# Kernel optimization log

Measured on AMD Instinct MI355X. Metric: run time of the kernel, lower is better.

## Reference

```python
import jax, jax.numpy as jnp
import numpy as np

E = 1024      # embed_dim
H = 16        # num_heads
D = E // H    # head_dim = 64
K = 4         # num_hyper_nodes
MAX_SEQ = 8192
ROPE_BASE = 10000.0
SCALE = D ** -0.5


def rotate_half(x):
    half = x.shape[-1] // 2
    return jnp.concatenate([-x[..., half:], x[..., :half]], axis=-1)


def _rope_cache():
    inv_freq = 1.0 / (ROPE_BASE ** (jnp.arange(0, D, 2, dtype=jnp.float32) / D))
    t = jnp.arange(MAX_SEQ, dtype=jnp.float32)
    freqs = jnp.outer(t, inv_freq)                       # (MAX_SEQ, D/2)
    emb = jnp.concatenate([freqs, freqs], axis=-1)       # (MAX_SEQ, D)
    return jnp.cos(emb), jnp.sin(emb)


def setup_inputs() -> dict:
    key = jax.random.key(0)
    ks = jax.random.split(key, 6)
    B, S = 2, 2048
    w_scale = E ** -0.5  # keep pre-softmax logits in a sane range
    return {
        "x":  jax.random.normal(ks[0], (B, S, E), dtype=jnp.float32),
        "Wq": jax.random.normal(ks[1], (E, E), dtype=jnp.float32) * w_scale,
        "Wk": jax.random.normal(ks[2], (E, E), dtype=jnp.float32) * w_scale,
        "Wv": jax.random.normal(ks[3], (E, E), dtype=jnp.float32) * w_scale,
        "Wr": jax.random.normal(ks[4], (E, H * K), dtype=jnp.float32) * w_scale,
        "Wo": jax.random.normal(ks[5], (E, E), dtype=jnp.float32) * w_scale,
    }


def reference(x, Wq, Wk, Wv, Wr, Wo):
    B, S, _ = x.shape
    # projections -> (B, H, S, D)
    q = (x @ Wq).reshape(B, S, H, D).transpose(0, 2, 1, 3)
    k = (x @ Wk).reshape(B, S, H, D).transpose(0, 2, 1, 3)
    v = (x @ Wv).reshape(B, S, H, D).transpose(0, 2, 1, 3)

    # node routing probabilities (B, H, S, K)
    logits = (x @ Wr).reshape(B, S, H, K).transpose(0, 2, 1, 3)
    node_probs = jax.nn.softmax(logits, axis=-1)

    # expected per-node position: sum_{j<i} p[j,k]  -> (B, H, S, K)
    expected_pos = jnp.cumsum(node_probs, axis=2) - node_probs

    # fractional-position RoPE via linear interpolation of the cos/sin cache
    cos_c, sin_c = _rope_cache()
    pos = jnp.clip(expected_pos, 0.0, MAX_SEQ - 1)
    pf = pos.astype(jnp.int32)                   # floor
    pc = jnp.minimum(pf + 1, MAX_SEQ - 1)        # ceil
    frac = (pos - pf.astype(pos.dtype))[..., None]
    cos = cos_c[pf] + frac * (cos_c[pc] - cos_c[pf])   # (B,H,S,K,D)
    sin = sin_c[pf] + frac * (sin_c[pc] - sin_c[pf])

    # Weighted combine over nodes. Since q_k = q*cos_k + rh(q)*sin_k is linear
    # in (cos_k, sin_k), sum_k p_k * q_k = q * (sum_k p_k cos_k) + rh(q) * (sum_k p_k sin_k)
    cos_w = jnp.einsum('bhsk,bhskd->bhsd', node_probs, cos)
    sin_w = jnp.einsum('bhsk,bhskd->bhsd', node_probs, sin)
    q_r = q * cos_w + rotate_half(q) * sin_w
    k_r = k * cos_w + rotate_half(k) * sin_w

    # P(same node) weights (B, H, S, S)
    node_w = jnp.einsum('bhik,bhjk->bhij', node_probs, node_probs)

    scores = jnp.einsum('bhid,bhjd->bhij', q_r, k_r) * SCALE
    scores = scores + jnp.log(node_w + 1e-8)
    causal = jnp.tril(jnp.ones((S, S), dtype=bool))
    scores = jnp.where(causal[None, None], scores, -jnp.inf)
    attn = jax.nn.softmax(scores, axis=-1)

    out = jnp.einsum('bhij,bhjd->bhid', attn, v)
    out = out.transpose(0, 2, 1, 3).reshape(B, S, E)
    return out @ Wo
```

## Files before the change

kernel.cpp:

```cpp
#include <hip/hip_runtime.h>

#define E_ 1024
#define H_ 16
#define D_ 64
#define K_ 4
#define S_ 2048
#define B_ 2
#define BS_ 4096
#define BH_ 32
#define CT_ 2080

typedef __attribute__((ext_vector_type(8))) short short8;
typedef __attribute__((ext_vector_type(4))) float f32x4;
typedef __attribute__((ext_vector_type(4))) unsigned short u16x4;

__device__ __forceinline__ unsigned short f2bf(float f) {
  union { float f; unsigned u; } v; v.f = f;
  unsigned r = v.u + 0x7FFFu + ((v.u >> 16) & 1u);
  return (unsigned short)(r >> 16);
}
__device__ __forceinline__ float bf2f(unsigned short u) {
  union { unsigned u; float f; } v; v.u = ((unsigned)u) << 16; return v.f;
}

typedef __attribute__((address_space(1))) const void gvoid;
typedef __attribute__((address_space(3))) void lvoid;
__device__ __forceinline__ void gload_lds16(const void* g, void* l) {
  __builtin_amdgcn_global_load_lds((gvoid*)g, (lvoid*)l, 16, 0, 0);
}

__device__ __forceinline__ short8 lds8(const unsigned short* base, int row, int chunk) {
  int off = row * 128 + (((chunk ^ (row & 7)) & 7) << 4);
  return *(const short8*)((const char*)base + off);
}

__device__ __forceinline__ float redmax16(float v) {
  int iv = __float_as_int(v);
  v = fmaxf(v, __int_as_float(__builtin_amdgcn_update_dpp(iv, iv, 0xB1, 0xF, 0xF, true)));
  iv = __float_as_int(v);
  v = fmaxf(v, __int_as_float(__builtin_amdgcn_update_dpp(iv, iv, 0x4E, 0xF, 0xF, true)));
  v = fmaxf(v, __shfl_xor(v, 4, 16));
  v = fmaxf(v, __shfl_xor(v, 8, 16));
  return v;
}

__global__ __launch_bounds__(256) void k_prep(const float* __restrict__ x,
    const float* __restrict__ Wq, const float* __restrict__ Wk, const float* __restrict__ Wv,
    const float* __restrict__ Wo, const float* __restrict__ Wr,
    unsigned short* __restrict__ xb, unsigned short* __restrict__ wt,
    float* __restrict__ cosc, float* __restrict__ sinc, float* __restrict__ logits) {
  __shared__ __align__(16) char smem[40960];
  int blk = blockIdx.x;
  int t = threadIdx.x;

  if (blk < 4096) {
    int i = blk * 256 + t;
    float4 v = ((const float4*)x)[i];
    u16x4 o; o.x = f2bf(v.x); o.y = f2bf(v.y); o.z = f2bf(v.z); o.w = f2bf(v.w);
    ((u16x4*)xb)[i] = o;
    return;
  }
  blk -= 4096;
  if (blk < 1024) {
    int z = blk >> 8, rem = blk & 255;
    int k0 = (rem >> 4) * 64, n0 = (rem & 15) * 64;
    const float* W = z == 0 ? Wq : z == 1 ? Wk : z == 2 ? Wv : Wo;
    unsigned short* out = wt + (size_t)z * E_ * E_;
    float (*tile)[65] = (float(*)[65])smem;
    int r = t >> 2, q4 = t & 3;
#pragma unroll
    for (int q = 0; q < 4; q++) {
      int c4 = q4 + q * 4;
      float4 v = *(const float4*)&W[(size_t)(k0 + r) * E_ + n0 + c4 * 4];
      tile[r][c4 * 4 + 0] = v.x; tile[r][c4 * 4 + 1] = v.y;
      tile[r][c4 * 4 + 2] = v.z; tile[r][c4 * 4 + 3] = v.w;
    }
    __syncthreads();
#pragma unroll
    for (int q = 0; q < 4; q++) {
      int cb = (q4 + q * 4) * 4;
      u16x4 o;
      o.x = f2bf(tile[cb + 0][r]); o.y = f2bf(tile[cb + 1][r]);
      o.z = f2bf(tile[cb + 2][r]); o.w = f2bf(tile[cb + 3][r]);
      *(u16x4*)&out[(size_t)(n0 + r) * E_ + k0 + cb] = o;
    }
    return;
  }
  blk -= 1024;
  if (blk < 260) {
    int i = blk * 256 + t;
    if (i < CT_ * 32) {
      int tt = i >> 5, f = i & 31;
      float invf = __expf(-(float)(2 * f) * (9.210340371976184f / 64.f));
      float ang = (float)tt * invf;
      cosc[i] = cosf(ang); sinc[i] = sinf(ang);
    }
    return;
  }
  blk -= 260;
  {
    float* xs = (float*)smem;
    float* ws = xs + 2048;
    int m0 = blk * 16;
    int r = t >> 4, cq = t & 15;
    f32x4 acc = {0.f, 0.f, 0.f, 0.f};

    auto stage = [&](int chunk, int buf) {
      int e0 = chunk * 64;
      gload_lds16(x + (size_t)(m0 + (t >> 4)) * E_ + e0 + (((t & 15) ^ (t >> 4)) << 2),
                  xs + buf * 1024 + t * 4);
#pragma unroll
      for (int j = 0; j < 4; j++) {
        int slot = j * 256 + t;
        gload_lds16(Wr + (size_t)(e0 + (slot >> 4)) * 64 + ((slot & 15) << 2),
                    ws + buf * 4096 + slot * 4);
      }
    };

    stage(0, 0);
    __syncthreads();
    for (int chunk = 0; chunk < 16; chunk++) {
      int cur = chunk & 1;
      if (chunk < 15) stage(chunk + 1, cur ^ 1);
#pragma unroll
      for (int e4 = 0; e4 < 16; e4++) {
        f32x4 xf = *(const f32x4*)(xs + cur * 1024 + (r * 16 + (e4 ^ r)) * 4);
#pragma unroll
        for (int i = 0; i < 4; i++) {
          f32x4 wf = *(const f32x4*)(ws + cur * 4096 + ((e4 * 4 + i) * 16 + cq) * 4);
          acc[0] = fmaf(xf[i], wf[0], acc[0]);
          acc[1] = fmaf(xf[i], wf[1], acc[1]);
          acc[2] = fmaf(xf[i], wf[2], acc[2]);
          acc[3] = fmaf(xf[i], wf[3], acc[3]);
        }
      }
      __syncthreads();
    }
    *(f32x4*)&logits[(size_t)(m0 + r) * 64 + cq * 4] = acc;
  }
}

__global__ __launch_bounds__(256) void k_scan1(const float* __restrict__ logits,
    float* __restrict__ probs, unsigned short* __restrict__ pb, float* __restrict__ eposl,
    float* __restrict__ chunkSum) {
  int g = blockIdx.x;
  int bh = g >> 3, c = g & 7;
  int b = bh >> 4, h = bh & 15;
  int t = threadIdx.x;
  int s = c * 256 + t;
  float4 lg = *(const float4*)&logits[(size_t)(b * S_ + s) * 64 + h * 4];
  float m = fmaxf(fmaxf(lg.x, lg.y), fmaxf(lg.z, lg.w));
  float e0 = __expf(lg.x - m), e1 = __expf(lg.y - m), e2 = __expf(lg.z - m), e3 = __expf(lg.w - m);
  float inv = 1.f / (e0 + e1 + e2 + e3);
  float p[4] = {e0 * inv, e1 * inv, e2 * inv, e3 * inv};
  float4 pv; pv.x = p[0]; pv.y = p[1]; pv.z = p[2]; pv.w = p[3];
  *(float4*)&probs[((size_t)bh * S_ + s) * 4] = pv;
  u16x4 pu; pu.x = f2bf(p[0]); pu.y = f2bf(p[1]); pu.z = f2bf(p[2]); pu.w = f2bf(p[3]);
  *(u16x4*)&pb[((size_t)bh * S_ + s) * 4] = pu;

  __shared__ float sc[4][256];
#pragma unroll
  for (int k = 0; k < 4; k++) sc[k][t] = p[k];
  __syncthreads();
  for (int off = 1; off < 256; off <<= 1) {
    float v0 = 0, v1 = 0, v2 = 0, v3 = 0;
    if (t >= off) { v0 = sc[0][t - off]; v1 = sc[1][t - off]; v2 = sc[2][t - off]; v3 = sc[3][t - off]; }
    __syncthreads();
    if (t >= off) { sc[0][t] += v0; sc[1][t] += v1; sc[2][t] += v2; sc[3][t] += v3; }
    __syncthreads();
  }
  float4 ev;
  ev.x = sc[0][t] - p[0]; ev.y = sc[1][t] - p[1];
  ev.z = sc[2][t] - p[2]; ev.w = sc[3][t] - p[3];
  *(float4*)&eposl[((size_t)bh * S_ + s) * 4] = ev;
  if (t == 255) {
    float4 cs; cs.x = sc[0][255]; cs.y = sc[1][255]; cs.z = sc[2][255]; cs.w = sc[3][255];
    *(float4*)&chunkSum[(size_t)(bh * 8 + c) * 4] = cs;
  }
}

__global__ __launch_bounds__(64) void k_scan2(const float* __restrict__ chunkSum,
    float* __restrict__ chunkBase) {
  int bh = threadIdx.x;
  if (bh >= 32) return;
  float r0 = 0.f, r1 = 0.f, r2 = 0.f, r3 = 0.f;
  for (int c = 0; c < 8; c++) {
    float4 cs = *(const float4*)&chunkSum[(size_t)(bh * 8 + c) * 4];
    float4 cb; cb.x = r0; cb.y = r1; cb.z = r2; cb.w = r3;
    *(float4*)&chunkBase[(size_t)(bh * 8 + c) * 4] = cb;
    r0 += cs.x; r1 += cs.y; r2 += cs.z; r3 += cs.w;
  }
}

__global__ __launch_bounds__(256) void k_cwsw(const float* __restrict__ probs,
    const float* __restrict__ eposl, const float* __restrict__ chunkBase,
    const float* __restrict__ cosc, const float* __restrict__ sinc,
    float* __restrict__ cw, float* __restrict__ sw) {
  int bh = blockIdx.y;
  int s = blockIdx.x * 8 + (threadIdx.x >> 5);
  int f = threadIdx.x & 31;
  size_t row = (size_t)bh * S_ + s;
  const float* cb = &chunkBase[(size_t)(bh * 8 + (s >> 8)) * 4];
  float cacc = 0.f, sacc = 0.f;
#pragma unroll
  for (int k = 0; k < 4; k++) {
    float pk = probs[row * 4 + k];
    float pos = eposl[row * 4 + k] + cb[k];
    pos = fminf(fmaxf(pos, 0.f), (float)(CT_ - 2));
    int pf = (int)pos; float fr = pos - (float)pf;
    float c0 = cosc[pf * 32 + f], c1 = cosc[pf * 32 + 32 + f];
    float s0 = sinc[pf * 32 + f], s1 = sinc[pf * 32 + 32 + f];
    cacc = fmaf(pk, c0 + fr * (c1 - c0), cacc);
    sacc = fmaf(pk, s0 + fr * (s1 - s0), sacc);
  }
  cw[row * 32 + f] = cacc; sw[row * 32 + f] = sacc;
}

__device__ __forceinline__ void gemm_128x128(const unsigned short* __restrict__ A,
    const unsigned short* __restrict__ Bt, int m0, int n0,
    unsigned short* lA, unsigned short* lB, f32x4 acc[4][4]) {
  int t = threadIdx.x, w = t >> 6, lane = t & 63;
  int wm = w >> 1, wn = w & 1;
  int arow = lane & 15, agrp = lane >> 4;
  for (int k0 = 0; k0 < E_; k0 += 64) {
    __syncthreads();
#pragma unroll
    for (int j = 0; j < 4; j++) {
      int c = j * 256 + w * 64 + lane;
      int row = c >> 3, slot = c & 7;
      gload_lds16(A + (size_t)(m0 + row) * E_ + k0 + ((slot ^ (row & 7)) << 3),
                  lA + (size_t)(j * 256 + w * 64) * 8);
      gload_lds16(Bt + (size_t)(n0 + row) * E_ + k0 + ((slot ^ (row & 7)) << 3),
                  lB + (size_t)(j * 256 + w * 64) * 8);
    }
    __syncthreads();
#pragma unroll
    for (int ks = 0; ks < 2; ks++) {
      short8 af[4], bfr[4];
#pragma unroll
      for (int mi = 0; mi < 4; mi++) af[mi] = lds8(lA, wm * 64 + mi * 16 + arow, ks * 4 + agrp);
#pragma unroll
      for (int nj = 0; nj < 4; nj++) bfr[nj] = lds8(lB, wn * 64 + nj * 16 + arow, ks * 4 + agrp);
#pragma unroll
      for (int mi = 0; mi < 4; mi++)
#pragma unroll
        for (int nj = 0; nj < 4; nj++)
          acc[mi][nj] = __builtin_amdgcn_mfma_f32_16x16x32_bf16(af[mi], bfr[nj], acc[mi][nj], 0, 0, 0);
    }
  }
}

__global__ __launch_bounds__(256) void k_gemm_qkv(const unsigned short* __restrict__ xb,
    const unsigned short* __restrict__ wt, const float* __restrict__ cw, const float* __restrict__ sw,
    unsigned short* __restrict__ qr, unsigned short* __restrict__ kr, unsigned short* __restrict__ vb) {
  __shared__ unsigned short lA[128 * 64], lB[128 * 64];
  int z = blockIdx.z;
  int m0 = blockIdx.y * 128, n0 = blockIdx.x * 128;
  f32x4 acc[4][4];
  f32x4 zero4 = {0.f, 0.f, 0.f, 0.f};
#pragma unroll
  for (int a = 0; a < 4; a++)
#pragma unroll
    for (int b2 = 0; b2 < 4; b2++) acc[a][b2] = zero4;
  gemm_128x128(xb, wt + (size_t)z * E_ * E_, m0, n0, lA, lB, acc);

  int t = threadIdx.x, w = t >> 6, lane = t & 63;
  int wm = w >> 1, wn = w & 1;
  int arow = lane & 15, agrp = lane >> 4;
  if (z == 2) {
#pragma unroll
    for (int mi = 0; mi < 4; mi++) {
      int i0 = m0 + wm * 64 + mi * 16 + agrp * 4;
      int b = i0 >> 11, s0 = i0 & 2047;
#pragma unroll
      for (int nj = 0; nj < 4; nj++) {
        int col = n0 + wn * 64 + nj * 16 + arow;
        int h = col >> 6, dl = col & 63;
        u16x4 o;
        o.x = f2bf(acc[mi][nj][0]); o.y = f2bf(acc[mi][nj][1]);
        o.z = f2bf(acc[mi][nj][2]); o.w = f2bf(acc[mi][nj][3]);
        *(u16x4*)&vb[((size_t)(b * H_ + h) * 64 + dl) * S_ + s0] = o;
      }
    }
  } else {
    unsigned short* out = (z == 0) ? qr : kr;
    float scl = (z == 0) ? 0.18033688011f : 1.0f;
    int h = (n0 + wn * 64) >> 6;
#pragma unroll
    for (int mi = 0; mi < 4; mi++)
#pragma unroll
      for (int reg = 0; reg < 4; reg++) {
        int i = m0 + wm * 64 + mi * 16 + agrp * 4 + reg;
        int b = i >> 11, s = i & 2047;
        size_t rbase = (size_t)(b * H_ + h) * S_ + s;
        float cw0 = cw[rbase * 32 + arow], cw1 = cw[rbase * 32 + 16 + arow];
        float sw0 = sw[rbase * 32 + arow], sw1 = sw[rbase * 32 + 16 + arow];
#pragma unroll
        for (int nj = 0; nj < 4; nj++) {
          float v = acc[mi][nj][reg];
          float part = acc[mi][nj ^ 2][reg];
          float rh = (nj < 2) ? -part : part;
          float cwv = (nj & 1) ? cw1 : cw0;
          float swv = (nj & 1) ? sw1 : sw0;
          out[rbase * 64 + nj * 16 + arow] = f2bf((v * cwv + rh * swv) * scl);
        }
      }
  }
}

__global__ __launch_bounds__(256) void k_gemm_out(const unsigned short* __restrict__ ob,
    const unsigned short* __restrict__ wot, float* __restrict__ dout) {
  __shared__ unsigned short lA[64 * 64];
  __shared__ unsigned short lB[128 * 64];
  int m0 = blockIdx.y * 64, n0 = blockIdx.x * 128;
  int t = threadIdx.x, w = t >> 6, lane = t & 63;
  int arow = lane & 15, agrp = lane >> 4;
  f32x4 acc[4][2];
  f32x4 zero4 = {0.f, 0.f, 0.f, 0.f};
#pragma unroll
  for (int a = 0; a < 4; a++) { acc[a][0] = zero4; acc[a][1] = zero4; }
  for (int k0 = 0; k0 < E_; k0 += 64) {
    __syncthreads();
#pragma unroll
    for (int j = 0; j < 2; j++) {
      int c = j * 256 + t;
      int row = c >> 3, slot = c & 7;
      gload_lds16(ob + (size_t)(m0 + row) * E_ + k0 + ((slot ^ (row & 7)) << 3),
                  lA + (size_t)c * 8);
    }
#pragma unroll
    for (int j = 0; j < 4; j++) {
      int c = j * 256 + t;
      int row = c >> 3, slot = c & 7;
      gload_lds16(wot + (size_t)(n0 + row) * E_ + k0 + ((slot ^ (row & 7)) << 3),
                  lB + (size_t)c * 8);
    }
    __syncthreads();
#pragma unroll
    for (int ks = 0; ks < 2; ks++) {
      short8 af[4], bfr[2];
#pragma unroll
      for (int mi = 0; mi < 4; mi++) af[mi] = lds8(lA, mi * 16 + arow, ks * 4 + agrp);
#pragma unroll
      for (int nj = 0; nj < 2; nj++) bfr[nj] = lds8(lB, w * 32 + nj * 16 + arow, ks * 4 + agrp);
#pragma unroll
      for (int mi = 0; mi < 4; mi++)
#pragma unroll
        for (int nj = 0; nj < 2; nj++)
          acc[mi][nj] = __builtin_amdgcn_mfma_f32_16x16x32_bf16(af[mi], bfr[nj], acc[mi][nj], 0, 0, 0);
    }
  }
#pragma unroll
  for (int mi = 0; mi < 4; mi++)
#pragma unroll
    for (int reg = 0; reg < 4; reg++) {
      int i = m0 + mi * 16 + agrp * 4 + reg;
#pragma unroll
      for (int nj = 0; nj < 2; nj++) {
        int col = n0 + w * 32 + nj * 16 + arow;
        dout[(size_t)i * E_ + col] = acc[mi][nj][reg];
      }
    }
}

__device__ const int4 kChunk[38] = {
  { 8,0, 8, 8},{ 8,9,17, 9},{12,0, 8,19},{12,9,17,20},
  { 7,0, 7, 6},{ 7,8,15, 7},{10,0, 7,13},{11,0, 7,16},{11,8,15,17},{11,16,23,18},
  {12,18,25,21},{14,0, 7,26},{14,8,15,27},{15,0, 7,30},{15,8,15,31},{15,16,23,32},
  {15,24,31,33},{ 3,0, 7,-1},
  { 6,0, 6, 4},{ 6,7,13, 5},{ 9,0, 6,10},{ 9,7,13,11},{10,8,14,14},{10,15,21,15},
  {13,0, 6,22},{13,7,13,23},{13,14,20,24},{13,21,27,25},{14,16,22,28},{14,23,29,29},
  { 5,0, 5, 2},{ 5,6,11, 3},{ 9,14,19,12},{ 2,0, 5,-1},
  { 4,0, 4, 0},{ 4,5, 9, 1},{ 1,0, 3,-1},{ 0,0, 1,-1}
};

__device__ __forceinline__ short8 mkfrag(u16x4 pv) {
  union { u16x4 v; unsigned u[2]; } pun; pun.v = pv;
  union { short8 s; unsigned u[4]; } z;
  z.u[0] = pun.u[0]; z.u[1] = pun.u[1]; z.u[2] = 0; z.u[3] = 0;
  return z.s;
}

__device__ __forceinline__ void qk_phase2(const char* lKc, const short8 qf[2][2],
    const int kOff[2][4], f32x4 zero4, f32x4 sacc[2][4]) {
#pragma unroll
  for (int ct = 0; ct < 4; ct++) {
    short8 kf = *(const short8*)(lKc + kOff[0][ct]);
    sacc[0][ct] = __builtin_amdgcn_mfma_f32_16x16x32_bf16(qf[0][0], kf, zero4, 0, 0, 0);
    sacc[1][ct] = __builtin_amdgcn_mfma_f32_16x16x32_bf16(qf[1][0], kf, zero4, 0, 0, 0);
  }
#pragma unroll
  for (int ct = 0; ct < 4; ct++) {
    short8 kf = *(const short8*)(lKc + kOff[1][ct]);
    sacc[0][ct] = __builtin_amdgcn_mfma_f32_16x16x32_bf16(qf[0][1], kf, sacc[0][ct], 0, 0, 0);
    sacc[1][ct] = __builtin_amdgcn_mfma_f32_16x16x32_bf16(qf[1][1], kf, sacc[1][ct], 0, 0, 0);
  }
}

__device__ __forceinline__ void softmax_half(const f32x4 sacc[4], const short8 piF,
    const short8 pjF[4], char* lPh, int kv0, int ig_base, int arow, int agrp,
    const int wOff[4][4], float mrow[4], f32x4 oacc[4], f32x4& o4) {
  f32x4 eps4 = {1e-8f, 1e-8f, 1e-8f, 1e-8f};
  f32x4 nwa[4];
#pragma unroll
  for (int ct = 0; ct < 4; ct++)
    nwa[ct] = __builtin_amdgcn_mfma_f32_16x16x32_bf16(piF, pjF[ct], eps4, 0, 0, 0);
  float sv[4][4];
  float rmax[4];
  if (kv0 + 63 > ig_base) {
#pragma unroll
    for (int ct = 0; ct < 4; ct++) {
      int jg = kv0 + ct * 16 + arow;
#pragma unroll
      for (int reg = 0; reg < 4; reg++) {
        int ig = ig_base + agrp * 4 + reg;
        float xv = sacc[ct][reg];
        if (jg > ig) xv = -1e30f;
        sv[ct][reg] = xv;
      }
    }
  } else {
#pragma unroll
    for (int ct = 0; ct < 4; ct++)
#pragma unroll
      for (int reg = 0; reg < 4; reg++)
        sv[ct][reg] = sacc[ct][reg];
  }
#pragma unroll
  for (int reg = 0; reg < 4; reg++)
    rmax[reg] = redmax16(fmaxf(fmaxf(sv[0][reg], sv[1][reg]), fmaxf(sv[2][reg], sv[3][reg])));
  bool ok = (rmax[0] <= mrow[0] + 11.5f) & (rmax[1] <= mrow[1] + 11.5f) &
            (rmax[2] <= mrow[2] + 11.5f) & (rmax[3] <= mrow[3] + 11.5f);
  if (!__all(ok)) {
    float alpha[4];
#pragma unroll
    for (int reg = 0; reg < 4; reg++) {
      float mn = fmaxf(mrow[reg], rmax[reg]);
      alpha[reg] = __builtin_amdgcn_exp2f(mrow[reg] - mn);
      mrow[reg] = mn;
    }
#pragma unroll
    for (int dt = 0; dt < 4; dt++) {
      f32x4 o = oacc[dt];
      o.x *= alpha[0]; o.y *= alpha[1]; o.z *= alpha[2]; o.w *= alpha[3];
      oacc[dt] = o;
    }
    o4.x *= alpha[0]; o4.y *= alpha[1]; o4.z *= alpha[2]; o4.w *= alpha[3];
  }
#pragma unroll
  for (int ct = 0; ct < 4; ct++)
#pragma unroll
    for (int reg = 0; reg < 4; reg++)
      sv[ct][reg] = __builtin_amdgcn_exp2f(sv[ct][reg] - mrow[reg]) * nwa[ct][reg];
#pragma unroll
  for (int ct = 0; ct < 4; ct++) {
#pragma unroll
    for (int rp = 0; rp < 2; rp++) {
      unsigned pk;
      asm("v_cvt_pk_bf16_f32 %0, %1, %2" : "=v"(pk) : "v"(sv[ct][rp * 2]), "v"(sv[ct][rp * 2 + 1]));
      *(unsigned short*)(lPh + wOff[ct][rp * 2 + 0]) = (unsigned short)pk;
      *(unsigned short*)(lPh + wOff[ct][rp * 2 + 1]) = (unsigned short)(pk >> 16);
    }
  }
}

__device__ __forceinline__ void pv2(const char* lPw, const char* lVc,
    const int pOff[2], const int kOff[2][4], f32x4 oacc0[4], f32x4 oacc1[4],
    f32x4& o40, f32x4& o41) {
  const short8 ones = {16256, 16256, 16256, 16256, 16256, 16256, 16256, 16256};
#pragma unroll
  for (int ks = 0; ks < 2; ks++) {
    short8 pf0 = *(const short8*)(lPw + pOff[ks]);
    short8 pf1 = *(const short8*)(lPw + 2048 + pOff[ks]);
    o40 = __builtin_amdgcn_mfma_f32_16x16x32_bf16(pf0, ones, o40, 0, 0, 0);
    o41 = __builtin_amdgcn_mfma_f32_16x16x32_bf16(pf1, ones, o41, 0, 0, 0);
#pragma unroll
    for (int dt = 0; dt < 4; dt++) {
      short8 vf = *(const short8*)(lVc + kOff[ks][dt]);
      oacc0[dt] = __builtin_amdgcn_mfma_f32_16x16x32_bf16(pf0, vf, oacc0[dt], 0, 0, 0);
      oacc1[dt] = __builtin_amdgcn_mfma_f32_16x16x32_bf16(pf1, vf, oacc1[dt], 0, 0, 0);
    }
  }
}

__global__ __launch_bounds__(256, 2) void k_attn(const unsigned short* __restrict__ qr,
    const unsigned short* __restrict__ kr, const unsigned short* __restrict__ vb,
    const unsigned short* __restrict__ pb, unsigned short* __restrict__ ob,
    unsigned short* __restrict__ ObP, float* __restrict__ ml) {
  __shared__ unsigned short lK[2][64 * 64];
  __shared__ unsigned short lV[2][64 * 64];
  __shared__ unsigned short lP[4][2][16 * 64];
  int id = blockIdx.x;
  int xcd = id & 7, slt = id >> 3;
  int bh = xcd * 4 + (slt & 3);
  int4 ck = kChunk[slt >> 2];
  int qt2 = ck.x, j0 = ck.y, j1 = ck.z, part = ck.w;
  int t = threadIdx.x, w = t >> 6, lane = t & 63;
  int arow = lane & 15, agrp = lane >> 4;
  int q0 = qt2 * 128;
  size_t base = (size_t)bh * S_ * 64;
  size_t bhS = (size_t)bh * S_;

  int kOff[2][4], pOff[2], wOff[4][4];
#pragma unroll
  for (int ks = 0; ks < 2; ks++) {
    pOff[ks] = arow * 128 + (((ks * 4 + agrp) ^ (arow & 7)) << 4);
#pragma unroll
    for (int ct = 0; ct < 4; ct++) {
      int row = ct * 16 + arow;
      kOff[ks][ct] = row * 128 + (((ks * 4 + agrp) ^ (row & 7)) << 4);
    }
  }
#pragma unroll
  for (int ct = 0; ct < 4; ct++) {
    int col2 = (ct * 16 + arow) * 2;
#pragma unroll
    for (int rr = 0; rr < 4; rr++) {
      int r = agrp * 4 + rr;
      wOff[ct][rr] = r * 128 + (col2 ^ ((r & 7) << 4));
    }
  }

  const unsigned short* kSrc[2];
  const unsigned short* vSrc[2];
  unsigned short* kDst[2];
  unsigned short* vDst[2];
#pragma unroll
  for (int j = 0; j < 2; j++) {
    int c = j * 256 + w * 64 + lane;
    int row = c >> 3, slot = c & 7;
    kSrc[j] = kr + base + (size_t)row * 64 + ((slot ^ (row & 7)) << 3);
    vSrc[j] = vb + base + (size_t)row * S_ + ((slot ^ (row & 7)) << 3);
    kDst[j] = &lK[0][(j * 256 + w * 64) * 8];
    vDst[j] = &lV[0][(j * 256 + w * 64) * 8];
  }
  const unsigned short* pjSrc[4];
#pragma unroll
  for (int ct = 0; ct < 4; ct++) pjSrc[ct] = pb + (bhS + ct * 16 + arow) * 4;

  short8 qf[2][2];
  short8 piF[2];
  float mrow[2][4];
  f32x4 oacc[2][4];
  f32x4 o4[2];
  f32x4 zero4 = {0.f, 0.f, 0.f, 0.f};
#pragma unroll
  for (int hh = 0; hh < 2; hh++) {
#pragma unroll
    for (int ks = 0; ks < 2; ks++)
      qf[hh][ks] = *(const short8*)&qr[base + (size_t)(q0 + hh * 64 + w * 16 + arow) * 64 + ks * 32 + agrp * 8];
    u16x4 pv = {0, 0, 0, 0};
    if (agrp == 0) pv = *(const u16x4*)&pb[(bhS + q0 + hh * 64 + w * 16 + arow) * 4];
    piF[hh] = mkfrag(pv);
#pragma unroll
    for (int reg = 0; reg < 4; reg++) mrow[hh][reg] = -1e30f;
#pragma unroll
    for (int dt = 0; dt < 4; dt++) oacc[hh][dt] = zero4;
    o4[hh] = zero4;
  }

  auto stageK = [&](int jt, int buf) {
#pragma unroll
    for (int j = 0; j < 2; j++)
      gload_lds16(kSrc[j] + jt * 4096, kDst[j] + buf * 4096);
  };
  auto stageV = [&](int jt, int buf) {
#pragma unroll
    for (int j = 0; j < 2; j++)
      gload_lds16(vSrc[j] + jt * 64, vDst[j] + buf * 4096);
  };
  auto loadPj = [&](int jt, u16x4 pj[4]) {
#pragma unroll
    for (int ct = 0; ct < 4; ct++) {
      u16x4 z = {0, 0, 0, 0};
      if (agrp == 0) z = *(const u16x4*)(pjSrc[ct] + jt * 256);
      pj[ct] = z;
    }
  };

  u16x4 pjv[4], pjvn[4];
  stageK(j0, 0);
  stageV(j0, 0);
  loadPj(j0, pjv);
  __syncthreads();

  char* lPw = (char*)&lP[w][0][0];
  int nt = j1 - j0 + 1;
  for (int i = 0; i < nt; i++) {
    int cur = i & 1;
    int kv0 = (j0 + i) * 64;
    bool hn = (i + 1) < nt;
    if (hn) {
      stageK(j0 + i + 1, cur ^ 1);
      stageV(j0 + i + 1, cur ^ 1);
    }

    f32x4 sacc[2][4];
    __builtin_amdgcn_s_setprio(1);
    qk_phase2((const char*)lK + cur * 8192, qf, kOff, zero4, sacc);
    __builtin_amdgcn_s_setprio(0);

    short8 pjF[4];
#pragma unroll
    for (int ct = 0; ct < 4; ct++) pjF[ct] = mkfrag(pjv[ct]);
#pragma unroll
    for (int hh = 0; hh < 2; hh++)
      softmax_half(sacc[hh], piF[hh], pjF, lPw + hh * 2048, kv0, q0 + hh * 64 + w * 16,
                   arow, agrp, wOff, mrow[hh], oacc[hh], o4[hh]);

    if (hn) loadPj(j0 + i + 1, pjvn);

    asm volatile("s_waitcnt lgkmcnt(0)" ::: "memory");
    __builtin_amdgcn_sched_barrier(0);
    __builtin_amdgcn_s_setprio(1);
    pv2(lPw, (const char*)lV + cur * 8192, pOff, kOff, oacc[0], oacc[1], o4[0], o4[1]);
    __builtin_amdgcn_s_setprio(0);
    if (hn) {
#pragma unroll
      for (int ct = 0; ct < 4; ct++) pjv[ct] = pjvn[ct];
    }
    __syncthreads();
  }

  if (part >= 0) {
    unsigned short* Op = ObP + ((size_t)bh * 34 + part) * 8192;
    float* mlp = ml + ((size_t)bh * 34 + part) * 256;
#pragma unroll
    for (int hh = 0; hh < 2; hh++) {
#pragma unroll
      for (int dt = 0; dt < 4; dt++)
#pragma unroll
        for (int reg = 0; reg < 4; reg++) {
          int row = hh * 64 + w * 16 + agrp * 4 + reg;
          Op[row * 64 + dt * 16 + arow] = f2bf(oacc[hh][dt][reg]);
        }
      if (arow == 0) {
#pragma unroll
        for (int reg = 0; reg < 4; reg++) {
          int row = hh * 64 + w * 16 + agrp * 4 + reg;
          mlp[row] = mrow[hh][reg];
          mlp[128 + row] = o4[hh][reg];
        }
      }
    }
  } else {
    int b = bh >> 4, h8 = bh & 15;
#pragma unroll
    for (int hh = 0; hh < 2; hh++) {
      f32x4 inv4;
      inv4.x = 1.f / o4[hh].x; inv4.y = 1.f / o4[hh].y;
      inv4.z = 1.f / o4[hh].z; inv4.w = 1.f / o4[hh].w;
#pragma unroll
      for (int dt = 0; dt < 4; dt++)
#pragma unroll
        for (int reg = 0; reg < 4; reg++) {
          int i = q0 + hh * 64 + w * 16 + agrp * 4 + reg;
          int d = dt * 16 + arow;
          float v = oacc[hh][dt][reg] * inv4[reg];
          ob[((size_t)(b * S_ + i) * H_ + h8) * 64 + d] = f2bf(v);
        }
    }
  }
}

__global__ __launch_bounds__(256) void k_merge(const unsigned short* __restrict__ ObP,
    const float* __restrict__ ml, unsigned short* __restrict__ ob) {
  int qx = blockIdx.x, bh = blockIdx.y;
  int qt2 = 4 + qx;
  int np = qt2 <= 8 ? 2 : (qt2 <= 12 ? 3 : 4);
  int bslot = qt2 <= 8 ? (qt2 - 4) * 2 : (qt2 <= 12 ? 10 + (qt2 - 9) * 3 : 22 + (qt2 - 13) * 4);
  int t = threadIdx.x;
  int r = t >> 1, dh = (t & 1) * 32;
  float mp[4], lp[4];
  float m = -1e30f;
  for (int p2 = 0; p2 < np; p2++) {
    const float* mlp = ml + ((size_t)bh * 34 + bslot + p2) * 256;
    mp[p2] = mlp[r]; lp[p2] = mlp[128 + r];
    m = fmaxf(m, mp[p2]);
  }
  float a[4], l = 0.f;
  for (int p2 = 0; p2 < np; p2++) { a[p2] = __builtin_amdgcn_exp2f(mp[p2] - m); l = fmaf(lp[p2], a[p2], l); }
  float inv = 1.f / l;
  for (int p2 = 0; p2 < np; p2++) a[p2] *= inv;
  int i = qt2 * 128 + r, b = bh >> 4, h = bh & 15;
  unsigned short* op = ob + ((size_t)(b * S_ + i) * H_ + h) * 64 + dh;
#pragma unroll
  for (int q = 0; q < 8; q++) {
    float a0 = 0.f, a1 = 0.f, a2 = 0.f, a3 = 0.f;
    for (int p2 = 0; p2 < np; p2++) {
      const unsigned short* Op = ObP + ((size_t)bh * 34 + bslot + p2) * 8192 + r * 64 + dh + q * 4;
      u16x4 xx = *(const u16x4*)Op;
      a0 = fmaf(bf2f(xx.x), a[p2], a0);
      a1 = fmaf(bf2f(xx.y), a[p2], a1);
      a2 = fmaf(bf2f(xx.z), a[p2], a2);
      a3 = fmaf(bf2f(xx.w), a[p2], a3);
    }
    u16x4 o; o.x = f2bf(a0); o.y = f2bf(a1); o.z = f2bf(a2); o.w = f2bf(a3);
    *(u16x4*)(op + q * 4) = o;
  }
}

extern "C" void kernel_launch(void* const* d_in, const int* in_sizes, int n_in,
                              void* d_out, int out_size, void* d_ws, size_t ws_size,
                              hipStream_t stream) {
  const float* x  = (const float*)d_in[0];
  const float* Wq = (const float*)d_in[1];
  const float* Wk = (const float*)d_in[2];
  const float* Wv = (const float*)d_in[3];
  const float* Wr = (const float*)d_in[4];
  const float* Wo = (const float*)d_in[5];
  float* dout = (float*)d_out;

  char* p = (char*)d_ws;
  auto alloc = [&](size_t bytes) -> char* {
    char* r = p; p += (bytes + 255) & ~(size_t)255; return r;
  };
  unsigned short* xb   = (unsigned short*)alloc((size_t)BS_ * E_ * 2);
  unsigned short* wt   = (unsigned short*)alloc((size_t)4 * E_ * E_ * 2);
  float* cosc          = (float*)alloc((size_t)CT_ * 32 * 4);
  float* sinc          = (float*)alloc((size_t)CT_ * 32 * 4);
  float* probs         = (float*)alloc((size_t)BH_ * S_ * 4 * 4);
  unsigned short* pb   = (unsigned short*)alloc((size_t)BH_ * S_ * 4 * 2);
  float* logits        = (float*)alloc((size_t)BS_ * 64 * 4);
  float* epos          = (float*)alloc((size_t)BH_ * S_ * 4 * 4);
  float* cw            = (float*)alloc((size_t)BH_ * S_ * 32 * 4);
  float* sw            = (float*)alloc((size_t)BH_ * S_ * 32 * 4);
  unsigned short* qrb  = (unsigned short*)alloc((size_t)BH_ * S_ * 64 * 2);
  unsigned short* krb  = (unsigned short*)alloc((size_t)BH_ * S_ * 64 * 2);
  unsigned short* vbb  = (unsigned short*)alloc((size_t)BH_ * S_ * 64 * 2);
  unsigned short* obb  = (unsigned short*)alloc((size_t)BS_ * E_ * 2);
  float* chunkSum      = (float*)alloc((size_t)BH_ * 8 * 4 * 4);
  float* chunkBase     = (float*)alloc((size_t)BH_ * 8 * 4 * 4);
  if ((size_t)(p - (char*)d_ws) > ws_size) return;

  unsigned short* ObP = (unsigned short*)logits;
  float* mlbuf = (float*)xb;

  k_prep<<<4096 + 1024 + 260 + 256, 256, 0, stream>>>(x, Wq, Wk, Wv, Wo, Wr,
                                                      xb, wt, cosc, sinc, logits);
  k_scan1<<<BH_ * 8, 256, 0, stream>>>(logits, probs, pb, epos, chunkSum);
  k_scan2<<<1, 64, 0, stream>>>(chunkSum, chunkBase);
  k_cwsw<<<dim3(S_ / 8, BH_), 256, 0, stream>>>(probs, epos, chunkBase, cosc, sinc, cw, sw);
  k_gemm_qkv<<<dim3(8, 32, 3), 256, 0, stream>>>(xb, wt, cw, sw, qrb, krb, vbb);
  k_attn<<<dim3(38 * BH_), 256, 0, stream>>>(qrb, krb, vbb, pb, obb, ObP, mlbuf);
  k_merge<<<dim3(12, BH_), 256, 0, stream>>>(ObP, mlbuf, obb);
  k_gemm_out<<<dim3(8, 64), 256, 0, stream>>>(obb, wt + (size_t)3 * E_ * E_, dout);
}
```

Before: 191.6 us.

## Software-pipeline QK of next tile with softmax and remap GEMM blocks per XCD

The attention loop is restructured so the QK^T scores for tile i+1 are computed before the softmax and PV of tile i. K is staged two tiles ahead and V one tile ahead, and the loop is unrolled by two with ping-pong score and Pj registers. This is meant to let MFMA work overlap the softmax ALU work. Separately, the QKV and output GEMMs remap block IDs so that consecutive M tiles land on the same XCD, which should improve L2 reuse. The cost is higher register pressure from the doubled score accumulators, which may reduce occupancy.

```diff
diff --git a/kernel.cpp b/kernel.cpp
--- a/kernel.cpp
+++ b/kernel.cpp
@@ -255,7 +255,11 @@
     unsigned short* __restrict__ qr, unsigned short* __restrict__ kr, unsigned short* __restrict__ vb) {
   __shared__ unsigned short lA[128 * 64], lB[128 * 64];
   int z = blockIdx.z;
-  int m0 = blockIdx.y * 128, n0 = blockIdx.x * 128;
+  int id = blockIdx.x + 8 * blockIdx.y;
+  int xcd = id & 7, slot = id >> 3;
+  int my = (xcd << 2) | (slot & 3);
+  int nx = slot >> 2;
+  int m0 = my * 128, n0 = nx * 128;
   f32x4 acc[4][4];
   f32x4 zero4 = {0.f, 0.f, 0.f, 0.f};
 #pragma unroll
@@ -312,7 +316,11 @@
     const unsigned short* __restrict__ wot, float* __restrict__ dout) {
   __shared__ unsigned short lA[64 * 64];
   __shared__ unsigned short lB[128 * 64];
-  int m0 = blockIdx.y * 64, n0 = blockIdx.x * 128;
+  int id = blockIdx.x + 8 * blockIdx.y;
+  int xcd = id & 7, slot = id >> 3;
+  int my = (xcd << 3) | (slot & 7);
+  int nx = slot >> 3;
+  int m0 = my * 64, n0 = nx * 128;
   int t = threadIdx.x, w = t >> 6, lane = t & 63;
   int arow = lane & 15, agrp = lane >> 4;
   f32x4 acc[4][2];
@@ -324,15 +332,15 @@
 #pragma unroll
     for (int j = 0; j < 2; j++) {
       int c = j * 256 + t;
-      int row = c >> 3, slot = c & 7;
-      gload_lds16(ob + (size_t)(m0 + row) * E_ + k0 + ((slot ^ (row & 7)) << 3),
+      int row = c >> 3, slot2 = c & 7;
+      gload_lds16(ob + (size_t)(m0 + row) * E_ + k0 + ((slot2 ^ (row & 7)) << 3),
                   lA + (size_t)c * 8);
     }
 #pragma unroll
     for (int j = 0; j < 4; j++) {
       int c = j * 256 + t;
-      int row = c >> 3, slot = c & 7;
-      gload_lds16(wot + (size_t)(n0 + row) * E_ + k0 + ((slot ^ (row & 7)) << 3),
+      int row = c >> 3, slot2 = c & 7;
+      gload_lds16(wot + (size_t)(n0 + row) * E_ + k0 + ((slot2 ^ (row & 7)) << 3),
                   lB + (size_t)c * 8);
     }
     __syncthreads();
@@ -578,49 +586,56 @@
     }
   };
 
-  u16x4 pjv[4], pjvn[4];
+  char* lPw = (char*)&lP[w][0][0];
+  int nt = j1 - j0 + 1;
+
+  f32x4 saccA[2][4], saccB[2][4];
+  u16x4 pjvA[4], pjvB[4];
+
   stageK(j0, 0);
   stageV(j0, 0);
-  loadPj(j0, pjv);
+  if (nt > 1) stageK(j0 + 1, 1);
+  loadPj(j0, pjvA);
   __syncthreads();
-
-  char* lPw = (char*)&lP[w][0][0];
-  int nt = j1 - j0 + 1;
-  for (int i = 0; i < nt; i++) {
-    int cur = i & 1;
-    int kv0 = (j0 + i) * 64;
-    bool hn = (i + 1) < nt;
-    if (hn) {
-      stageK(j0 + i + 1, cur ^ 1);
-      stageV(j0 + i + 1, cur ^ 1);
-    }
-
-    f32x4 sacc[2][4];
-    __builtin_amdgcn_s_setprio(1);
-    qk_phase2((const char*)lK + cur * 8192, qf, kOff, zero4, sacc);
-    __builtin_amdgcn_s_setprio(0);
-
-    short8 pjF[4];
-#pragma unroll
-    for (int ct = 0; ct < 4; ct++) pjF[ct] = mkfrag(pjv[ct]);
-#pragma unroll
-    for (int hh = 0; hh < 2; hh++)
-      softmax_half(sacc[hh], piF[hh], pjF, lPw + hh * 2048, kv0, q0 + hh * 64 + w * 16,
-                   arow, agrp, wOff, mrow[hh], oacc[hh], o4[hh]);
-
-    if (hn) loadPj(j0 + i + 1, pjvn);
-
-    asm volatile("s_waitcnt lgkmcnt(0)" ::: "memory");
-    __builtin_amdgcn_sched_barrier(0);
-    __builtin_amdgcn_s_setprio(1);
-    pv2(lPw, (const char*)lV + cur * 8192, pOff, kOff, oacc[0], oacc[1], o4[0], o4[1]);
-    __builtin_amdgcn_s_setprio(0);
-    if (hn) {
-#pragma unroll
-      for (int ct = 0; ct < 4; ct++) pjv[ct] = pjvn[ct];
-    }
-    __syncthreads();
-  }
+  qk_phase2((const char*)lK, qf, kOff, zero4, saccA);
+
+#define ATTN_BODY(i_, scC, scN, pjC, pjN)                                       \
+  {                                                                             \
+    int cur = (i_) & 1;                                                         \
+    int kv0 = (j0 + (i_)) * 64;                                                 \
+    __syncthreads();                                                            \
+    if ((i_) + 2 < nt) stageK(j0 + (i_) + 2, cur);                              \
+    if ((i_) + 1 < nt) {                                                        \
+      stageV(j0 + (i_) + 1, cur ^ 1);                                           \
+      qk_phase2((const char*)lK + (cur ^ 1) * 8192, qf, kOff, zero4, scN);      \
+    }                                                                           \
+    short8 pjF[4];                                                              \
+    _Pragma("unroll")                                                           \
+    for (int ct = 0; ct < 4; ct++) pjF[ct] = mkfrag(pjC[ct]);                   \
+    _Pragma("unroll")                                                           \
+    for (int hh = 0; hh < 2; hh++)                                              \
+      softmax_half(scC[hh], piF[hh], pjF, lPw + hh * 2048, kv0,                 \
+                   q0 + hh * 64 + w * 16, arow, agrp, wOff, mrow[hh],           \
+                   oacc[hh], o4[hh]);                                           \
+    if ((i_) + 1 < nt) loadPj(j0 + (i_) + 1, pjN);                              \
+    asm volatile("s_waitcnt lgkmcnt(0)" ::: "memory");                          \
+    __builtin_amdgcn_sched_barrier(0);                                          \
+    __builtin_amdgcn_s_setprio(1);                                              \
+    pv2(lPw, (const char*)lV + cur * 8192, pOff, kOff, oacc[0], oacc[1],        \
+        o4[0], o4[1]);                                                          \
+    __builtin_amdgcn_s_setprio(0);                                              \
+  }
+
+  {
+    int i = 0;
+    for (;;) {
+      ATTN_BODY(i, saccA, saccB, pjvA, pjvB);
+      if (++i >= nt) break;
+      ATTN_BODY(i, saccB, saccA, pjvB, pjvA);
+      if (++i >= nt) break;
+    }
+  }
+#undef ATTN_BODY
 
   if (part >= 0) {
     unsigned short* Op = ObP + ((size_t)bh * 34 + part) * 8192;
```

Result: slower. 201.5 us (+5.2%).
